# Kernel tuning notes

Measured on AMD Instinct MI355X. Metric: run time of the kernel, lower is better.

The kernel has to match this reference:

```python
import jax, jax.numpy as jnp
import numpy as np

T, B, F, H, C = 128, 64, 512, 1024, 513


def _tess_big(W):
    # W: (4, d_in/4, d_out/4) components (r, i, j, k).
    # Tessarine product (commutative): i^2=-1, j^2=+1, k=ij, k^2=-1.
    # Equivalent real block matrix so x @ bigW computes the tessarine linear.
    Wr, Wi, Wj, Wk = W[0], W[1], W[2], W[3]
    return jnp.concatenate([
        jnp.concatenate([Wr,  Wi,  Wj,  Wk], axis=1),
        jnp.concatenate([-Wi, Wr, -Wk,  Wj], axis=1),
        jnp.concatenate([Wj,  Wk,  Wr,  Wi], axis=1),
        jnp.concatenate([-Wk, Wj, -Wi,  Wr], axis=1),
    ], axis=0)  # (d_in, d_out)


def setup_inputs() -> dict:
    key = jax.random.key(0)
    ks = jax.random.split(key, 16)

    def w(k, din, dout):
        return (jax.random.normal(k, (4, din // 4, dout // 4), jnp.float32)
                / np.float32(np.sqrt(din)))

    return {
        "x": jax.random.normal(ks[0], (T, B, F), jnp.float32),
        "wfx_W": w(ks[1], F, H), "wfx_b": jnp.zeros((H,), jnp.float32),
        "wfh_W": w(ks[2], H, H),
        "wix_W": w(ks[3], F, H), "wix_b": jnp.zeros((H,), jnp.float32),
        "wih_W": w(ks[4], H, H),
        "wox_W": w(ks[5], F, H), "wox_b": jnp.zeros((H,), jnp.float32),
        "woh_W": w(ks[6], H, H),
        "wcx_W": w(ks[7], F, H), "wcx_b": jnp.zeros((H,), jnp.float32),
        "wch_W": w(ks[8], H, H),
        "fco_W": jax.random.normal(ks[9], (H, C), jnp.float32) / np.float32(np.sqrt(H)),
        "fco_b": jnp.zeros((C,), jnp.float32),
    }


def reference(x, wfx_W, wfx_b, wfh_W, wix_W, wix_b, wih_W,
              wox_W, wox_b, woh_W, wcx_W, wcx_b, wch_W, fco_W, fco_b):
    Tn, Bn, _ = x.shape
    Hd = wfh_W.shape[1] * 4

    # Precompute input-to-hidden tessarine linears for all timesteps: (T, B, H)
    gx_f = x @ _tess_big(wfx_W) + wfx_b
    gx_i = x @ _tess_big(wix_W) + wix_b
    gx_o = x @ _tess_big(wox_W) + wox_b
    gx_c = x @ _tess_big(wcx_W) + wcx_b

    Wfh = _tess_big(wfh_W)
    Wih = _tess_big(wih_W)
    Woh = _tess_big(woh_W)
    Wch = _tess_big(wch_W)

    def step(carry, g):
        h, c = carry
        fx, ix, ox, cx = g
        ft = jax.nn.sigmoid(fx + h @ Wfh)
        it = jax.nn.sigmoid(ix + h @ Wih)
        ot = jax.nn.sigmoid(ox + h @ Woh)
        at = cx + h @ Wch
        c = it * jnp.tanh(at) + ft * c
        h = ot * jnp.tanh(c)
        return (h, c), None

    h0 = jnp.zeros((Bn, Hd), x.dtype)
    (h, _), _ = jax.lax.scan(step, (h0, h0), (gx_f, gx_i, gx_o, gx_c))
    return h @ fco_W + fco_b  # (B, num_classes)
```

## Files before the change

kernel.cpp:

```cpp
#include <hip/hip_runtime.h>
#include <hip/hip_cooperative_groups.h>

typedef short bfv8 __attribute__((ext_vector_type(8)));
typedef float fv4  __attribute__((ext_vector_type(4)));
typedef unsigned long long u64;

#define T_STEPS 128
#define BATCH   64
#define FDIM    512
#define HDIM    1024
#define NCLS    513
#define HSLOT   65536

#define PREP_N0V 524288
#define PREP_N1  2097152
#define PREP_N2  4194304
#define PREP_N3  4096
#define PREP_N4V 8192
#define PREP_N5  4096
#define PREP_N6  525312
#define PREP_TOTAL (PREP_N0V + PREP_N1 + PREP_N2 + PREP_N3 + PREP_N4V + PREP_N5 + PREP_N6)

static __device__ __forceinline__ float b2f(unsigned short u) {
  union { unsigned int i; float f; } v; v.i = ((unsigned int)u) << 16; return v.f;
}
static __device__ __forceinline__ unsigned short f2b(float f) {
  union { float f; unsigned int i; } v; v.f = f;
  unsigned int r = v.i + 0x7FFFu + ((v.i >> 16) & 1u);
  return (unsigned short)(r >> 16);
}
static __device__ __forceinline__ float sigm(float x) { return 1.0f / (1.0f + __expf(-x)); }
static __device__ __forceinline__ float tanh_f(float x) {
  float e = __expf(-2.0f * fabsf(x));
  float t = (1.0f - e) / (1.0f + e);
  return x >= 0.0f ? t : -t;
}

static __device__ __forceinline__ int detect_fl(const void* __restrict__ x, int lane) {
  unsigned short ux = ((const unsigned short*)x)[2 * lane];
  int ex = (ux >> 7) & 0xFF;
  u64 bal = __ballot(ex >= 112 && ex <= 131);
  return (__builtin_popcountll(bal) >= 32) ? 1 : 0;
}

__global__ void prep_k(const void* __restrict__ x,
                       const void* w0x, const void* w1x, const void* w2x, const void* w3x,
                       const void* w0h, const void* w1h, const void* w2h, const void* w3h,
                       const void* b0, const void* b1, const void* b2, const void* b3,
                       const void* __restrict__ fcw,
                       unsigned short* __restrict__ xbf,
                       unsigned short* __restrict__ WXT,
                       unsigned short* __restrict__ WHT,
                       float* __restrict__ biasI,
                       unsigned short* __restrict__ hring0,
                       int* __restrict__ flags,
                       float* __restrict__ fcwT) {
  int fl = detect_fl(x, threadIdx.x & 63);
  long idx = (long)blockIdx.x * 256 + threadIdx.x;
  if (idx < PREP_N0V) {
    int i = (int)idx * 8;
    if (fl) {
      *(uint4*)&xbf[i] = *(const uint4*)&((const unsigned short*)x)[i];
    } else {
      const float* xf = (const float*)x;
      union { unsigned short s[8]; uint4 q; } o;
#pragma unroll
      for (int e = 0; e < 8; ++e) o.s[e] = f2b(xf[i + e]);
      *(uint4*)&xbf[i] = o.q;
    }
    return;
  }
  idx -= PREP_N0V;
  if (idx < PREP_N1) {
    int i = (int)idx;
    int n = i >> 9, k = i & 511;
    int j = n >> 2, g = n & 3;
    int rb = k >> 7, p = k & 127;
    int cb = j >> 8, q = j & 255;
    int comp = rb ^ cb;
    int neg = (rb & 1) && !(cb & 1);
    const void* W = (g == 0) ? w0x : (g == 1) ? w1x : (g == 2) ? w2x : w3x;
    int off = comp * (128 * 256) + p * 256 + q;
    unsigned short v;
    if (fl) { v = ((const unsigned short*)W)[off]; if (neg) v ^= 0x8000u; }
    else    { float f = ((const float*)W)[off]; if (neg) f = -f; v = f2b(f); }
    WXT[i] = v;
    return;
  }
  idx -= PREP_N1;
  if (idx < PREP_N2) {
    int i = (int)idx;
    int n = i >> 10, k = i & 1023;
    int j = n >> 2, g = n & 3;
    int rb = k >> 8, p = k & 255;
    int cb = j >> 8, q = j & 255;
    int comp = rb ^ cb;
    int neg = (rb & 1) && !(cb & 1);
    const void* W = (g == 0) ? w0h : (g == 1) ? w1h : (g == 2) ? w2h : w3h;
    int off = comp * (256 * 256) + p * 256 + q;
    unsigned short v;
    if (fl) { v = ((const unsigned short*)W)[off]; if (neg) v ^= 0x8000u; }
    else    { float f = ((const float*)W)[off]; if (neg) f = -f; v = f2b(f); }
    WHT[i] = v;
    return;
  }
  idx -= PREP_N2;
  if (idx < PREP_N3) {
    int i = (int)idx;
    int j = i >> 2, g = i & 3;
    const void* B = (g == 0) ? b0 : (g == 1) ? b1 : (g == 2) ? b2 : b3;
    biasI[i] = fl ? b2f(((const unsigned short*)B)[j]) : ((const float*)B)[j];
    return;
  }
  idx -= PREP_N3;
  if (idx < PREP_N4V) {
    uint4 z = {0u, 0u, 0u, 0u};
    *(uint4*)&hring0[(int)idx * 8] = z;
    return;
  }
  idx -= PREP_N4V;
  if (idx < PREP_N5) { flags[(int)idx] = 0; return; }
  idx -= PREP_N5;
  {
    int i = (int)idx;
    int col = i >> 10, k = i & 1023;
    float v = fl ? b2f(((const unsigned short*)fcw)[k * NCLS + col])
                 : ((const float*)fcw)[k * NCLS + col];
    fcwT[col * 1024 + k] = v;
  }
}

static __device__ __forceinline__ float dot512T(const unsigned short* __restrict__ hfin,
                                                const float* __restrict__ fcwT,
                                                int b, int col, int half) {
  const float* wcol = fcwT + (size_t)col * 1024 + half * 512;
  float s0 = 0.f, s1 = 0.f, s2 = 0.f, s3 = 0.f;
#pragma unroll 4
  for (int c = 0; c < 32; ++c) {
    int k16 = half * 32 + c;
    const unsigned short* hp = hfin + k16 * 256 + b * 16;
    bfv8 h0 = *(const bfv8*)hp;
    bfv8 h1 = *(const bfv8*)(hp + 8);
    const float4* wp = (const float4*)(wcol + c * 16);
    float4 w0 = wp[0], w1 = wp[1], w2 = wp[2], w3 = wp[3];
    s0 = fmaf(b2f((unsigned short)h0[0]), w0.x, s0);
    s1 = fmaf(b2f((unsigned short)h0[1]), w0.y, s1);
    s2 = fmaf(b2f((unsigned short)h0[2]), w0.z, s2);
    s3 = fmaf(b2f((unsigned short)h0[3]), w0.w, s3);
    s0 = fmaf(b2f((unsigned short)h0[4]), w1.x, s0);
    s1 = fmaf(b2f((unsigned short)h0[5]), w1.y, s1);
    s2 = fmaf(b2f((unsigned short)h0[6]), w1.z, s2);
    s3 = fmaf(b2f((unsigned short)h0[7]), w1.w, s3);
    s0 = fmaf(b2f((unsigned short)h1[0]), w2.x, s0);
    s1 = fmaf(b2f((unsigned short)h1[1]), w2.y, s1);
    s2 = fmaf(b2f((unsigned short)h1[2]), w2.z, s2);
    s3 = fmaf(b2f((unsigned short)h1[3]), w2.w, s3);
    s0 = fmaf(b2f((unsigned short)h1[4]), w3.x, s0);
    s1 = fmaf(b2f((unsigned short)h1[5]), w3.y, s1);
    s2 = fmaf(b2f((unsigned short)h1[6]), w3.z, s2);
    s3 = fmaf(b2f((unsigned short)h1[7]), w3.w, s3);
  }
  return (s0 + s1) + (s2 + s3);
}

__global__ void __launch_bounds__(256, 1) phaseB_k(const void* __restrict__ xraw,
                                                   const unsigned short* __restrict__ xbf,
                                                   const unsigned short* __restrict__ WXT,
                                                   const unsigned short* __restrict__ WHT,
                                                   const float* __restrict__ biasI,
                                                   unsigned short* __restrict__ hring,
                                                   int* __restrict__ flags,
                                                   const float* __restrict__ fcwT,
                                                   const void* __restrict__ fcb,
                                                   void* __restrict__ out) {
  __shared__ unsigned short Wh[64][1032];
  __shared__ float Pl[4][16][16];
  __shared__ __align__(16) unsigned short Hp[16][16];
  __shared__ float Cred[128];
  int tid = threadIdx.x;
  int w = tid >> 6, lane = tid & 63;
  int fl = detect_fl(xraw, lane);
  int grp = blockIdx.x >> 6;
  int blk = blockIdx.x & 63;
  int n0  = blk * 64;
  for (int c = tid; c < 64 * 128; c += 256) {
    int row = c >> 7, ch = c & 127;
    *(uint4*)&Wh[row][ch * 8] = *(const uint4*)&WHT[(size_t)(n0 + row) * HDIM + ch * 8];
  }
  __syncthreads();
  int col = lane & 15, quad = lane >> 4;
  int gbatch = grp * 16 + col;
  const unsigned short* whp = &Wh[w * 16 + col][quad * 8];
  const unsigned short* wxp = WXT + (size_t)(n0 + w * 16 + col) * FDIM + quad * 8;
  float4 bv = *(const float4*)&biasI[n0 + w * 16 + quad * 4];
  int* myflag   = flags + (grp * 64 + blk) * 16;
  int* pollflag = flags + (grp * 64 + lane) * 16;
  size_t fbase = (size_t)grp * 16384 + (size_t)(quad >> 1) * 256
               + (size_t)col * 16 + (size_t)(quad & 1) * 8;
  size_t pregion = (size_t)grp * 16384 + (size_t)blk * 256;
  float creg = 0.0f;
  fv4 gx0 = {0.f, 0.f, 0.f, 0.f}, gx1 = {0.f, 0.f, 0.f, 0.f};
  {
    const unsigned short* xrow = xbf + (size_t)gbatch * FDIM + quad * 8;
#pragma unroll
    for (int k0 = 0; k0 < FDIM; k0 += 64) {
      bfv8 a0 = *(const bfv8*)(xrow + k0);
      bfv8 b0 = *(const bfv8*)(wxp + k0);
      bfv8 a1 = *(const bfv8*)(xrow + k0 + 32);
      bfv8 b1 = *(const bfv8*)(wxp + k0 + 32);
      gx0 = __builtin_amdgcn_mfma_f32_16x16x32_bf16(a0, b0, gx0, 0, 0, 0);
      gx1 = __builtin_amdgcn_mfma_f32_16x16x32_bf16(a1, b1, gx1, 0, 0, 0);
    }
  }
  for (int t = 0; t < T_STEPS; ++t) {
    const unsigned short* hin  = hring + (size_t)t * HSLOT;
    unsigned short*       hout = hring + (size_t)(t + 1) * HSLOT;
    const uint4* hq = (const uint4*)(hin + fbase);
    uint4 hs[32];
#pragma unroll
    for (int f = 0; f < 32; ++f) hs[f] = hq[f * 64];
    if (w == 0 && t > 0) {
      fv4 g0 = {0.f, 0.f, 0.f, 0.f}, g1 = {0.f, 0.f, 0.f, 0.f};
      const unsigned short* xrow = xbf + (size_t)(t * BATCH + gbatch) * FDIM + quad * 8;
#pragma unroll
      for (int k0 = 0; k0 < FDIM; k0 += 64) {
        bfv8 a0v = *(const bfv8*)(xrow + k0);
        bfv8 b0v = *(const bfv8*)(wxp + k0);
        bfv8 a1v = *(const bfv8*)(xrow + k0 + 32);
        bfv8 b1v = *(const bfv8*)(wxp + k0 + 32);
        g0 = __builtin_amdgcn_mfma_f32_16x16x32_bf16(a0v, b0v, g0, 0, 0, 0);
        g1 = __builtin_amdgcn_mfma_f32_16x16x32_bf16(a1v, b1v, g1, 0, 0, 0);
      }
      gx0 = g0; gx1 = g1;
    }
    fv4 acc0 = gx0, acc1 = gx1;
#pragma unroll
    for (int f = 0; f < 32; f += 2) {
      union { uint4 q; bfv8 v; } ua, ub;
      ua.q = hs[f];
      ub.q = hs[f + 1];
      bfv8 b0 = *(const bfv8*)(whp + f * 32);
      bfv8 b1 = *(const bfv8*)(whp + (f + 1) * 32);
      acc0 = __builtin_amdgcn_mfma_f32_16x16x32_bf16(ua.v, b0, acc0, 0, 0, 0);
      acc1 = __builtin_amdgcn_mfma_f32_16x16x32_bf16(ub.v, b1, acc1, 0, 0, 0);
    }
    fv4 acc = acc0 + acc1;
#pragma unroll
    for (int r = 0; r < 4; ++r) Pl[w][quad * 4 + r][col] = acc[r];
    asm volatile("" ::: "memory");
    __builtin_amdgcn_s_waitcnt(0);
    asm volatile("" ::: "memory");
    float4 pv = *(const float4*)&Pl[w][col][quad * 4];
    float fg = sigm(pv.x + bv.x);
    float ig = sigm(pv.y + bv.y);
    float og = sigm(pv.z + bv.z);
    float av = pv.w + bv.w;
    float cn = ig * tanh_f(av) + fg * creg;
    float hn = og * tanh_f(cn);
    creg = cn;
    Hp[col][w * 4 + quad] = f2b(hn);
    __syncthreads();
    if (w == 0) {
      u64 pk = ((const u64*)&Hp[0][0])[lane];
      __hip_atomic_store((u64*)(hout + pregion) + lane, pk,
                         __ATOMIC_RELAXED, __HIP_MEMORY_SCOPE_AGENT);
    }
    if (t + 1 < T_STEPS) {
      if (w == 0) {
        asm volatile("s_waitcnt vmcnt(0)" ::: "memory");
        if (lane == 0)
          __hip_atomic_store(myflag, t + 1, __ATOMIC_RELAXED, __HIP_MEMORY_SCOPE_AGENT);
      } else {
        fv4 g0 = {0.f, 0.f, 0.f, 0.f}, g1 = {0.f, 0.f, 0.f, 0.f};
        const unsigned short* xrow = xbf + (size_t)((t + 1) * BATCH + gbatch) * FDIM + quad * 8;
#pragma unroll
        for (int k0 = 0; k0 < FDIM; k0 += 64) {
          bfv8 a0v = *(const bfv8*)(xrow + k0);
          bfv8 b0v = *(const bfv8*)(wxp + k0);
          bfv8 a1v = *(const bfv8*)(xrow + k0 + 32);
          bfv8 b1v = *(const bfv8*)(wxp + k0 + 32);
          g0 = __builtin_amdgcn_mfma_f32_16x16x32_bf16(a0v, b0v, g0, 0, 0, 0);
          g1 = __builtin_amdgcn_mfma_f32_16x16x32_bf16(a1v, b1v, g1, 0, 0, 0);
        }
        gx0 = g0; gx1 = g1;
      }
      asm volatile("" ::: "memory");
      u64 done = 0;
      for (;;) {
        int v = 0;
        if (!((done >> lane) & 1))
          v = __hip_atomic_load(pollflag, __ATOMIC_RELAXED, __HIP_MEMORY_SCOPE_AGENT);
        done |= __ballot(v >= t + 1);
        if (done == ~0ull) break;
        __builtin_amdgcn_s_sleep(1);
      }
      asm volatile("" ::: "memory");
    }
  }
  if (w == 0) {
    asm volatile("s_waitcnt vmcnt(0)" ::: "memory");
    if (lane == 0)
      __hip_atomic_store(myflag, T_STEPS, __ATOMIC_RELAXED, __HIP_MEMORY_SCOPE_AGENT);
  }
  {
    u64 done = 0;
    for (;;) {
      int v = 0;
      if (!((done >> lane) & 1))
        v = __hip_atomic_load(pollflag, __ATOMIC_RELAXED, __HIP_MEMORY_SCOPE_AGENT);
      done |= __ballot(v >= T_STEPS);
      if (done == ~0ull) break;
      __builtin_amdgcn_s_sleep(1);
    }
  }
  asm volatile("" ::: "memory");
  {
    const unsigned short* hfin = hring + (size_t)T_STEPS * HSLOT + (size_t)grp * 16384;
    int b    = tid & 15;
    int cc   = (tid >> 4) & 7;
    int half = tid >> 7;
    int colm = blk * 8 + cc;
    float s = dot512T(hfin, fcwT, b, colm, half);
    if (half) Cred[tid & 127] = s;
    __syncthreads();
    if (!half) {
      float r = s + Cred[tid];
      float bias = fl ? b2f(((const unsigned short*)fcb)[colm])
                      : ((const float*)fcb)[colm];
      r += bias;
      int oidx = (grp * 16 + b) * NCLS + colm;
      if (fl) ((unsigned short*)out)[oidx] = f2b(r);
      else    ((float*)out)[oidx] = r;
    }
    if (blk == 63) {
      float s2 = 0.f;
      if (tid < 32) s2 = dot512T(hfin, fcwT, tid & 15, 512, tid >> 4);
      __syncthreads();
      if (tid < 32 && (tid >> 4)) Cred[tid & 15] = s2;
      __syncthreads();
      if (tid < 16) {
        float r = s2 + Cred[tid];
        r += fl ? b2f(((const unsigned short*)fcb)[512]) : ((const float*)fcb)[512];
        int oidx = (grp * 16 + tid) * NCLS + 512;
        if (fl) ((unsigned short*)out)[oidx] = f2b(r);
        else    ((float*)out)[oidx] = r;
      }
    }
  }
}

extern "C" void kernel_launch(void* const* d_in, const int* in_sizes, int n_in,
                              void* d_out, int out_size, void* d_ws, size_t ws_size,
                              hipStream_t stream) {
  const void* x   = d_in[0];
  const void* wfx = d_in[1];  const void* bfv = d_in[2];  const void* wfh = d_in[3];
  const void* wix = d_in[4];  const void* biv = d_in[5];  const void* wih = d_in[6];
  const void* wox = d_in[7];  const void* bov = d_in[8];  const void* woh = d_in[9];
  const void* wcx = d_in[10]; const void* bcv = d_in[11]; const void* wch = d_in[12];
  const void* fcw = d_in[13]; const void* fcb = d_in[14];

  char* ws = (char*)d_ws;
  unsigned short* WXT   = (unsigned short*)(ws + 256);
  unsigned short* WHT   = (unsigned short*)(ws + 4194560);
  float*          biasI = (float*)         (ws + 12583168);
  unsigned short* xbf   = (unsigned short*)(ws + 12599552);
  unsigned short* hring = (unsigned short*)(ws + 20988160);
  int*            flags = (int*)           (ws + 37896448);
  float*          fcwT  = (float*)         (ws + 37912832);

  prep_k<<<PREP_TOTAL / 256, 256, 0, stream>>>(x, wfx, wix, wox, wcx,
                                               wfh, wih, woh, wch,
                                               bfv, biv, bov, bcv, fcw,
                                               xbf, WXT, WHT, biasI,
                                               hring, flags, fcwT);

  phaseB_k<<<256, 256, 0, stream>>>(x, xbf, WXT, WHT, biasI, hring, flags,
                                    fcwT, fcb, d_out);
}
```

Baseline: 844.3 us.

## Split recurrent matmul over K across warps and prefetch x rows

Each warp now computes partial products for all four 16-column tiles over its own quarter of the hidden dimension, instead of the full K=1024 for one tile. Partial sums go through shared memory, are reduced after a block barrier, and then feed the gate math. Each warp therefore loads only 8 h fragments per step rather than 32, which shortens the serial load-to-MFMA chain on the critical recurrence path. Warp 0 also preloads its next-step x row into registers while it waits. The cost is a larger shared buffer, an extra __syncthreads and cross-warp reductions each step.

```diff
diff --git a/kernel.cpp b/kernel.cpp
--- a/kernel.cpp
+++ b/kernel.cpp
@@ -174,7 +174,7 @@
                                                    const void* __restrict__ fcb,
                                                    void* __restrict__ out) {
   __shared__ unsigned short Wh[64][1032];
-  __shared__ float Pl[4][16][16];
+  __shared__ float Pt[4][4][16][16];
   __shared__ __align__(16) unsigned short Hp[16][16];
   __shared__ float Cred[128];
   int tid = threadIdx.x;
@@ -190,7 +190,7 @@
   __syncthreads();
   int col = lane & 15, quad = lane >> 4;
   int gbatch = grp * 16 + col;
-  const unsigned short* whp = &Wh[w * 16 + col][quad * 8];
+  const unsigned short* whb = &Wh[col][w * 256 + quad * 8];
   const unsigned short* wxp = WXT + (size_t)(n0 + w * 16 + col) * FDIM + quad * 8;
   float4 bv = *(const float4*)&biasI[n0 + w * 16 + quad * 4];
   int* myflag   = flags + (grp * 64 + blk) * 16;
@@ -199,8 +199,10 @@
                + (size_t)col * 16 + (size_t)(quad & 1) * 8;
   size_t pregion = (size_t)grp * 16384 + (size_t)blk * 256;
   float creg = 0.0f;
-  fv4 gx0 = {0.f, 0.f, 0.f, 0.f}, gx1 = {0.f, 0.f, 0.f, 0.f};
+  uint4 xr[16];
+  fv4 gxs;
   {
+    fv4 g0 = {0.f, 0.f, 0.f, 0.f}, g1 = {0.f, 0.f, 0.f, 0.f};
     const unsigned short* xrow = xbf + (size_t)gbatch * FDIM + quad * 8;
 #pragma unroll
     for (int k0 = 0; k0 < FDIM; k0 += 64) {
@@ -208,53 +210,65 @@
       bfv8 b0 = *(const bfv8*)(wxp + k0);
       bfv8 a1 = *(const bfv8*)(xrow + k0 + 32);
       bfv8 b1 = *(const bfv8*)(wxp + k0 + 32);
-      gx0 = __builtin_amdgcn_mfma_f32_16x16x32_bf16(a0, b0, gx0, 0, 0, 0);
-      gx1 = __builtin_amdgcn_mfma_f32_16x16x32_bf16(a1, b1, gx1, 0, 0, 0);
-    }
+      g0 = __builtin_amdgcn_mfma_f32_16x16x32_bf16(a0, b0, g0, 0, 0, 0);
+      g1 = __builtin_amdgcn_mfma_f32_16x16x32_bf16(a1, b1, g1, 0, 0, 0);
+    }
+    gxs = g0 + g1;
   }
   for (int t = 0; t < T_STEPS; ++t) {
     const unsigned short* hin  = hring + (size_t)t * HSLOT;
     unsigned short*       hout = hring + (size_t)(t + 1) * HSLOT;
     const uint4* hq = (const uint4*)(hin + fbase);
-    uint4 hs[32];
-#pragma unroll
-    for (int f = 0; f < 32; ++f) hs[f] = hq[f * 64];
+    uint4 hs[8];
+#pragma unroll
+    for (int kk = 0; kk < 8; ++kk) hs[kk] = hq[(w * 8 + kk) * 64];
     if (w == 0 && t > 0) {
       fv4 g0 = {0.f, 0.f, 0.f, 0.f}, g1 = {0.f, 0.f, 0.f, 0.f};
-      const unsigned short* xrow = xbf + (size_t)(t * BATCH + gbatch) * FDIM + quad * 8;
-#pragma unroll
-      for (int k0 = 0; k0 < FDIM; k0 += 64) {
-        bfv8 a0v = *(const bfv8*)(xrow + k0);
-        bfv8 b0v = *(const bfv8*)(wxp + k0);
-        bfv8 a1v = *(const bfv8*)(xrow + k0 + 32);
-        bfv8 b1v = *(const bfv8*)(wxp + k0 + 32);
-        g0 = __builtin_amdgcn_mfma_f32_16x16x32_bf16(a0v, b0v, g0, 0, 0, 0);
-        g1 = __builtin_amdgcn_mfma_f32_16x16x32_bf16(a1v, b1v, g1, 0, 0, 0);
+#pragma unroll
+      for (int f = 0; f < 16; f += 2) {
+        union { uint4 q; bfv8 v; } u0, u1;
+        u0.q = xr[f]; u1.q = xr[f + 1];
+        bfv8 b0 = *(const bfv8*)(wxp + f * 32);
+        bfv8 b1 = *(const bfv8*)(wxp + (f + 1) * 32);
+        g0 = __builtin_amdgcn_mfma_f32_16x16x32_bf16(u0.v, b0, g0, 0, 0, 0);
+        g1 = __builtin_amdgcn_mfma_f32_16x16x32_bf16(u1.v, b1, g1, 0, 0, 0);
       }
-      gx0 = g0; gx1 = g1;
-    }
-    fv4 acc0 = gx0, acc1 = gx1;
-#pragma unroll
-    for (int f = 0; f < 32; f += 2) {
-      union { uint4 q; bfv8 v; } ua, ub;
-      ua.q = hs[f];
-      ub.q = hs[f + 1];
-      bfv8 b0 = *(const bfv8*)(whp + f * 32);
-      bfv8 b1 = *(const bfv8*)(whp + (f + 1) * 32);
-      acc0 = __builtin_amdgcn_mfma_f32_16x16x32_bf16(ua.v, b0, acc0, 0, 0, 0);
-      acc1 = __builtin_amdgcn_mfma_f32_16x16x32_bf16(ub.v, b1, acc1, 0, 0, 0);
-    }
-    fv4 acc = acc0 + acc1;
-#pragma unroll
-    for (int r = 0; r < 4; ++r) Pl[w][quad * 4 + r][col] = acc[r];
-    asm volatile("" ::: "memory");
-    __builtin_amdgcn_s_waitcnt(0);
-    asm volatile("" ::: "memory");
-    float4 pv = *(const float4*)&Pl[w][col][quad * 4];
-    float fg = sigm(pv.x + bv.x);
-    float ig = sigm(pv.y + bv.y);
-    float og = sigm(pv.z + bv.z);
-    float av = pv.w + bv.w;
+      gxs = g0 + g1;
+    }
+    fv4 a0 = {0.f, 0.f, 0.f, 0.f}, a1 = {0.f, 0.f, 0.f, 0.f};
+    fv4 a2 = {0.f, 0.f, 0.f, 0.f}, a3 = {0.f, 0.f, 0.f, 0.f};
+#pragma unroll
+    for (int kk = 0; kk < 8; ++kk) {
+      union { uint4 q; bfv8 v; } ua; ua.q = hs[kk];
+      bfv8 b0 = *(const bfv8*)(whb + kk * 32);
+      bfv8 b1 = *(const bfv8*)(whb + 16 * 1032 + kk * 32);
+      bfv8 b2 = *(const bfv8*)(whb + 32 * 1032 + kk * 32);
+      bfv8 b3 = *(const bfv8*)(whb + 48 * 1032 + kk * 32);
+      a0 = __builtin_amdgcn_mfma_f32_16x16x32_bf16(ua.v, b0, a0, 0, 0, 0);
+      a1 = __builtin_amdgcn_mfma_f32_16x16x32_bf16(ua.v, b1, a1, 0, 0, 0);
+      a2 = __builtin_amdgcn_mfma_f32_16x16x32_bf16(ua.v, b2, a2, 0, 0, 0);
+      a3 = __builtin_amdgcn_mfma_f32_16x16x32_bf16(ua.v, b3, a3, 0, 0, 0);
+    }
+    if      (w == 0) a0 = a0 + gxs;
+    else if (w == 1) a1 = a1 + gxs;
+    else if (w == 2) a2 = a2 + gxs;
+    else             a3 = a3 + gxs;
+#pragma unroll
+    for (int r = 0; r < 4; ++r) {
+      Pt[w][0][quad * 4 + r][col] = a0[r];
+      Pt[w][1][quad * 4 + r][col] = a1[r];
+      Pt[w][2][quad * 4 + r][col] = a2[r];
+      Pt[w][3][quad * 4 + r][col] = a3[r];
+    }
+    __syncthreads();
+    float4 p0 = *(const float4*)&Pt[0][w][col][quad * 4];
+    float4 p1 = *(const float4*)&Pt[1][w][col][quad * 4];
+    float4 p2 = *(const float4*)&Pt[2][w][col][quad * 4];
+    float4 p3 = *(const float4*)&Pt[3][w][col][quad * 4];
+    float fg = sigm((p0.x + p1.x) + (p2.x + p3.x) + bv.x);
+    float ig = sigm((p0.y + p1.y) + (p2.y + p3.y) + bv.y);
+    float og = sigm((p0.z + p1.z) + (p2.z + p3.z) + bv.z);
+    float av = (p0.w + p1.w) + (p2.w + p3.w) + bv.w;
     float cn = ig * tanh_f(av) + fg * creg;
     float hn = og * tanh_f(cn);
     creg = cn;
@@ -270,6 +284,9 @@
         asm volatile("s_waitcnt vmcnt(0)" ::: "memory");
         if (lane == 0)
           __hip_atomic_store(myflag, t + 1, __ATOMIC_RELAXED, __HIP_MEMORY_SCOPE_AGENT);
+        const unsigned short* xrow = xbf + (size_t)((t + 1) * BATCH + gbatch) * FDIM + quad * 8;
+#pragma unroll
+        for (int f = 0; f < 16; ++f) xr[f] = *(const uint4*)(xrow + f * 32);
       } else {
         fv4 g0 = {0.f, 0.f, 0.f, 0.f}, g1 = {0.f, 0.f, 0.f, 0.f};
         const unsigned short* xrow = xbf + (size_t)((t + 1) * BATCH + gbatch) * FDIM + quad * 8;
@@ -282,7 +299,7 @@
           g0 = __builtin_amdgcn_mfma_f32_16x16x32_bf16(a0v, b0v, g0, 0, 0, 0);
           g1 = __builtin_amdgcn_mfma_f32_16x16x32_bf16(a1v, b1v, g1, 0, 0, 0);
         }
-        gx0 = g0; gx1 = g1;
+        gxs = g0 + g1;
       }
       asm volatile("" ::: "memory");
       u64 done = 0;
```

After: 818.8 us (median of 2 runs). 3.0% less time.
